# Kernel optimization log

Measured on AMD Instinct MI355X. Metric: run time of the kernel, lower is better.

Reference implementation:

```python
import jax, jax.numpy as jnp
import numpy as np

COMMITMENT_COST = 0.25
EPS = 1e-10


def setup_inputs() -> dict:
    key = jax.random.key(0)
    k1, k2 = jax.random.split(key)
    z = jax.random.normal(k1, (8, 2048, 512), dtype=jnp.float32)
    # codebook ~ small uniform init in torch; small normal is fine for a numeric reference
    codebook = jax.random.normal(k2, (4096, 512), dtype=jnp.float32) * 0.02
    return {"z": z, "codebook": codebook}


def reference(z, codebook):
    B, S, D = z.shape
    K = codebook.shape[0]
    flat_z = z.reshape(-1, D)  # [N, D]
    distances = (
        jnp.sum(flat_z * flat_z, axis=1, keepdims=True)
        + jnp.sum(codebook * codebook, axis=1)
        - 2.0 * flat_z @ codebook.T
    )
    encoding_indices = jnp.argmin(distances, axis=1)  # [N] int
    z_q = codebook[encoding_indices].reshape(z.shape)  # gather lookup
    # commitment loss (z_q detached)
    commitment_loss = jnp.mean((z - jax.lax.stop_gradient(z_q)) ** 2)
    loss = COMMITMENT_COST * commitment_loss
    # straight-through estimator
    z_q_st = z + jax.lax.stop_gradient(z_q - z)
    # perplexity from codebook usage histogram
    N = flat_z.shape[0]
    counts = jnp.zeros((K,), dtype=jnp.float32).at[encoding_indices].add(1.0)
    avg_probs = counts / N
    perplexity = jnp.exp(-jnp.sum(avg_probs * jnp.log(avg_probs + EPS)))
    encoding_indices = encoding_indices.reshape(B, S)
    return (z_q_st, loss, encoding_indices, perplexity)
```

## Files before the change

kernel.cpp:

```cpp
#include <hip/hip_runtime.h>
#include <hip/hip_fp16.h>
#include <stdint.h>

#define B_  8
#define S_  2048
#define D_  512
#define K_  4096
#define N_  (B_ * S_)
#define NCB (K_ / 128)
#define NKB32 (D_ / 32)
#define MARGIN 0.014f

typedef _Float16 half8  __attribute__((ext_vector_type(8)));
typedef float    floatx4 __attribute__((ext_vector_type(4)));

#define OFF_PK   0
#define OFF_EN   (OFF_PK + (size_t)N_ * NCB * 8)
#define OFF_ZN   (OFF_EN + K_ * 4)
#define OFF_CNT  (OFF_ZN + N_ * 4)
#define OFF_BL   (OFF_CNT + K_ * 4)
#define OFF_ZH   (OFF_BL + 4096 * 4)
#define OFF_EH   (OFF_ZH + (size_t)N_ * D_ * 2)

__device__ __forceinline__ uint32_t umin32(uint32_t a, uint32_t b) { return a < b ? a : b; }
__device__ __forceinline__ uint32_t umax32(uint32_t a, uint32_t b) { return a > b ? a : b; }
__device__ __forceinline__ bool lexlt(float va, int ia, float vb, int ib) {
    return va < vb || (va == vb && ia < ib);
}

__device__ __forceinline__ void load_lds16(const _Float16* g, _Float16* l) {
    __builtin_amdgcn_global_load_lds(
        (const __attribute__((address_space(1))) unsigned int*)(uintptr_t)g,
        (__attribute__((address_space(3))) unsigned int*)(uintptr_t)l,
        16, 0, 0);
}

__global__ __launch_bounds__(256)
void vq_prep_kernel(const float* __restrict__ z, const float* __restrict__ cb,
                    _Float16* __restrict__ zh, _Float16* __restrict__ eh,
                    float* __restrict__ znorm, float* __restrict__ enorm,
                    int* __restrict__ counts) {
    const int t = threadIdx.x;
    if (blockIdx.x < 16) counts[blockIdx.x * 256 + t] = 0;

    const size_t u = (size_t)blockIdx.x * 256 + t;
    const int c   = (int)(u & 63);
    const int row = (int)(u >> 6);
    const bool isZ = row < N_;
    const int n = isZ ? row : row - N_;
    const float* r = (isZ ? z : cb) + (size_t)n * D_;

    float s = 0.f;
    for (int j = c; j < D_; j += 64) { float v = r[j]; s += v * v; }
    #pragma unroll
    for (int m = 1; m < 64; m <<= 1) s += __shfl_xor(s, m, 64);
    if (c == 0) { if (isZ) znorm[n] = s; else enorm[n] = s; }

    const float scale = isZ ? 1.0f : 64.0f;
    const float4 v0 = *(const float4*)(r + c * 8);
    const float4 v1 = *(const float4*)(r + c * 8 + 4);
    float a[8] = {v0.x, v0.y, v0.z, v0.w, v1.x, v1.y, v1.z, v1.w};
    half8 h;
    #pragma unroll
    for (int j = 0; j < 8; j++) h[j] = (_Float16)(a[j] * scale);
    const int kb = c >> 2, qd = c & 3;
    const int sw = qd ^ ((n >> 1) & 3);
    const size_t rows = isZ ? (size_t)N_ : (size_t)K_;
    const size_t off = (size_t)kb * rows * 32 + (size_t)n * 32 + (size_t)(sw << 3);
    *(half8*)((isZ ? zh : eh) + off) = h;
}

__global__ __launch_bounds__(256, 4)
void vq_dist_kernel(const _Float16* __restrict__ zh, const _Float16* __restrict__ eh,
                    const float* __restrict__ enorm, const float* __restrict__ znorm,
                    uint2* __restrict__ pK) {
    __shared__ _Float16 sA[2][4096];
    __shared__ float sE[128], sZn[128];
    __shared__ uint2 cK[2][128];

    const int t  = threadIdx.x;
    const int c0 = blockIdx.x * 128;
    const int m0 = blockIdx.y * 128;

    if (t < 128) { sE[t] = enorm[c0 + t]; sZn[t] = znorm[m0 + t]; }

    const int lane = t & 63, wid = t >> 6;
    const int wr = wid & 1, wc = wid >> 1;
    const int qd = lane >> 4, nl = lane & 15;
    const int sw8 = (qd ^ ((nl >> 1) & 3)) << 3;

    const _Float16* gsrc = zh + (size_t)m0 * 32 + (size_t)(wid * 2) * 512 + (size_t)lane * 8;
    const size_t strideA = (size_t)N_ * 32;
    const size_t strideB = (size_t)K_ * 32;
    const _Float16* bptr = eh + (size_t)c0 * 32 + (size_t)((wc * 64 + nl) * 32 + sw8);
    const int aoff = (wr * 64 + nl) * 32 + sw8;

    floatx4 acc[4][4];
    #pragma unroll
    for (int i = 0; i < 4; i++)
        #pragma unroll
        for (int j = 0; j < 4; j++) acc[i][j] = (floatx4)0.f;

    #pragma unroll
    for (int g = 0; g < 2; g++)
        load_lds16(gsrc + g * 512, sA[0] + wid * 2 * 512 + g * 512);

    for (int kb = 0; kb < NKB32; kb++) {
        __syncthreads();

        half8 b_h[4];
        #pragma unroll
        for (int s = 0; s < 4; s++)
            b_h[s] = *(const half8*)(bptr + s * 512);
        if (kb + 1 < NKB32) {
            const _Float16* gk = gsrc + (size_t)(kb + 1) * strideA;
            _Float16* ld = sA[(kb + 1) & 1] + wid * 2 * 512;
            #pragma unroll
            for (int g = 0; g < 2; g++)
                load_lds16(gk + g * 512, ld + g * 512);
        }
        const _Float16* ah = sA[kb & 1] + aoff;
        half8 a_h[4];
        #pragma unroll
        for (int s = 0; s < 4; s++)
            a_h[s] = *(const half8*)(ah + s * 512);
        #pragma unroll
        for (int i = 0; i < 4; i++)
            #pragma unroll
            for (int j = 0; j < 4; j++)
                acc[i][j] = __builtin_amdgcn_mfma_f32_16x16x32_f16(a_h[i], b_h[j], acc[i][j], 0, 0, 0);
        bptr += strideB;
    }

    uint32_t colc[4]; float se4[4];
    #pragma unroll
    for (int sn = 0; sn < 4; sn++) {
        const int cl = wc * 64 + sn * 16 + nl;
        colc[sn] = (uint32_t)cl;
        se4[sn]  = sE[cl];
    }
    #pragma unroll
    for (int sm = 0; sm < 4; sm++) {
        #pragma unroll
        for (int reg = 0; reg < 4; reg++) {
            const int rm = wr * 64 + sm * 16 + qd * 4 + reg;
            const float zn = sZn[rm];
            uint32_t k0 = 0xFFFFFFFFu, k1 = 0xFFFFFFFFu;
            #pragma unroll
            for (int sn = 0; sn < 4; sn++) {
                const float v = fmaf(acc[sm][sn][reg], -0.03125f, zn + se4[sn]);
                const uint32_t key = (__float_as_uint(v) & 0xFFFFFF80u) | colc[sn];
                const uint32_t t1 = umax32(k0, key);
                k1 = umin32(k1, t1);
                k0 = umin32(k0, key);
            }
            #pragma unroll
            for (int msk = 1; msk <= 8; msk <<= 1) {
                const uint32_t o0 = (uint32_t)__shfl_xor((int)k0, msk, 64);
                const uint32_t o1 = (uint32_t)__shfl_xor((int)k1, msk, 64);
                const uint32_t n0 = umin32(k0, o0);
                k1 = umin32(umax32(k0, o0), umin32(k1, o1));
                k0 = n0;
            }
            if (nl == 0) { cK[wc][rm].x = k0; cK[wc][rm].y = k1; }
        }
    }
    __syncthreads();
    if (t < 128) {
        const uint2 a = cK[0][t], b = cK[1][t];
        uint2 r;
        r.x = umin32(a.x, b.x);
        r.y = umin32(umax32(a.x, b.x), umin32(a.y, b.y));
        pK[(size_t)(m0 + t) * NCB + blockIdx.x] = r;
    }
}

__global__ __launch_bounds__(256)
void vq_gather_kernel(const float* __restrict__ z, const float* __restrict__ cb,
                      const float* __restrict__ znorm, const float* __restrict__ enorm,
                      const uint2* __restrict__ pK,
                      float* __restrict__ out_zq, float* __restrict__ out_idx,
                      int* __restrict__ counts, float* __restrict__ blockLoss) {
    const int lane = threadIdx.x & 63, wid = threadIdx.x >> 6;
    const int m = blockIdx.x * 4 + wid;

    uint32_t k0 = 0xFFFFFFFFu, k1 = 0xFFFFFFFFu;
    if (lane < NCB) {
        const uint2 kk = pK[(size_t)m * NCB + lane];
        k0 = kk.x; k1 = kk.y;
    }
    uint32_t g = k0;
    #pragma unroll
    for (int msk = 1; msk < 64; msk <<= 1) {
        const uint32_t o = (uint32_t)__shfl_xor((int)g, msk, 64);
        g = umin32(g, o);
    }
    const float gvf = __uint_as_float(g & 0xFFFFFF80u) + MARGIN;
    const bool f0 = (lane < NCB) && (__uint_as_float(k0 & 0xFFFFFF80u) <= gvf);
    const bool f1 = (lane < NCB) && (__uint_as_float(k1 & 0xFFFFFF80u) <= gvf);
    const unsigned long long b0 = __ballot(f0), b1 = __ballot(f1);
    int idx;
    if (__popcll(b0) + __popcll(b1) <= 1) {
        const unsigned long long bw = __ballot(k0 == g);
        idx = (int)__builtin_ctzll(bw) * 128 + (int)(g & 0x7Fu);
    } else {
        const float zn = znorm[m];
        const float* zrow = z + (size_t)m * D_;
        float bestd = 1e30f; int besti = 0x7fffffff;
        #pragma unroll
        for (int slot = 0; slot < 2; slot++) {
            unsigned long long bm = slot ? b1 : b0;
            while (bm) {
                const int l = (int)__builtin_ctzll(bm); bm &= bm - 1;
                const uint32_t kx = (uint32_t)__shfl((int)(slot ? k1 : k0), l, 64);
                const int cand = l * 128 + (int)(kx & 0x7Fu);
                const float* crow = cb + (size_t)cand * D_;
                float s = 0.f;
                #pragma unroll
                for (int j = 0; j < 8; j++)
                    s += zrow[lane * 8 + j] * crow[lane * 8 + j];
                #pragma unroll
                for (int msk = 1; msk < 64; msk <<= 1) s += __shfl_xor(s, msk, 64);
                const float d = (zn + enorm[cand]) - 2.0f * s;
                if (lexlt(d, cand, bestd, besti)) { bestd = d; besti = cand; }
            }
        }
        idx = besti;
    }

    const float4* qrow  = (const float4*)(cb + (size_t)idx * D_);
    const float4* zrow4 = (const float4*)(z + (size_t)m * D_);
    float4*       orow  = (float4*)(out_zq + (size_t)m * D_);
    float lsum = 0.f;
    #pragma unroll
    for (int i = 0; i < 2; i++) {
        const int j = lane + i * 64;
        const float4 q  = qrow[j];
        const float4 zv = zrow4[j];
        float4 o;
        o.x = zv.x + (q.x - zv.x); o.y = zv.y + (q.y - zv.y);
        o.z = zv.z + (q.z - zv.z); o.w = zv.w + (q.w - zv.w);
        orow[j] = o;
        const float dx = zv.x - q.x, dy = zv.y - q.y, dz = zv.z - q.z, dw = zv.w - q.w;
        lsum += dx * dx + dy * dy + dz * dz + dw * dw;
    }
    #pragma unroll
    for (int msk = 1; msk < 64; msk <<= 1) lsum += __shfl_xor(lsum, msk, 64);

    if (lane == 0) {
        out_idx[m] = (float)idx;
        atomicAdd(&counts[idx], 1);
    }
    __shared__ float wl[4];
    if (lane == 0) wl[wid] = lsum;
    __syncthreads();
    if (threadIdx.x == 0) blockLoss[blockIdx.x] = wl[0] + wl[1] + wl[2] + wl[3];
}

__global__ void vq_final_kernel(const int* __restrict__ counts,
                                const float* __restrict__ blockLoss,
                                float* __restrict__ out_loss, float* __restrict__ out_ppl) {
    __shared__ float sl[256], se[256];
    const int t = threadIdx.x;
    float ls = 0.f, es = 0.f;
    for (int i = t; i < N_ / 4; i += 256) ls += blockLoss[i];
    for (int k = t; k < K_; k += 256) {
        const float p = (float)counts[k] / (float)N_;
        es += p * logf(p + 1e-10f);
    }
    sl[t] = ls; se[t] = es;
    __syncthreads();
    for (int s = 128; s > 0; s >>= 1) {
        if (t < s) { sl[t] += sl[t + s]; se[t] += se[t + s]; }
        __syncthreads();
    }
    if (t == 0) {
        out_loss[0] = 0.25f * (sl[0] / (float)((size_t)N_ * D_));
        out_ppl[0]  = expf(-se[0]);
    }
}

extern "C" void kernel_launch(void* const* d_in, const int* in_sizes, int n_in,
                              void* d_out, int out_size, void* d_ws, size_t ws_size,
                              hipStream_t stream) {
    const float* z  = (const float*)d_in[0];
    const float* cb = (const float*)d_in[1];
    float* out = (float*)d_out;

    char* ws = (char*)d_ws;
    uint2*    pK        = (uint2*)   (ws + OFF_PK);
    float*    enorm     = (float*)   (ws + OFF_EN);
    float*    znorm     = (float*)   (ws + OFF_ZN);
    int*      counts    = (int*)     (ws + OFF_CNT);
    float*    blockLoss = (float*)   (ws + OFF_BL);
    _Float16* zh        = (_Float16*)(ws + OFF_ZH);
    _Float16* eh        = (_Float16*)(ws + OFF_EH);

    float* out_zq   = out;
    float* out_loss = out + (size_t)N_ * D_;
    float* out_idx  = out_loss + 1;
    float* out_ppl  = out_idx + N_;

    vq_prep_kernel<<<(N_ + K_) * 64 / 256, 256, 0, stream>>>(z, cb, zh, eh,
                                                             znorm, enorm, counts);

    dim3 grid(K_ / 128, N_ / 128);
    vq_dist_kernel<<<grid, 256, 0, stream>>>(zh, eh, enorm, znorm, pK);

    vq_gather_kernel<<<N_ / 4, 256, 0, stream>>>(z, cb, znorm, enorm, pK,
                                                 out_zq, out_idx, counts, blockLoss);

    vq_final_kernel<<<1, 256, 0, stream>>>(counts, blockLoss, out_loss, out_ppl);
}
```

Baseline: 205.2 us.

## Enlarge distance GEMM block tile to 256x256 with 1024-thread workgroups

The distance kernel now uses 1024-thread workgroups, each covering a 256x256 tile of rows by codes instead of 128x128. The per-wave 64x64 sub-tile and MFMA loop stay the same. The larger tile lets each block share more staged z data in LDS and reduces the number of blocks. Partial top-2 keys are still written per 128-column chunk, so the layout the gather kernel reads does not change. The trade-off is fewer, larger workgroups: one workgroup per CU by launch bounds, a block-wide barrier across 16 waves every k-step, and possibly worse latency hiding or tail balance.

```diff
diff --git a/kernel.cpp b/kernel.cpp
--- a/kernel.cpp
+++ b/kernel.cpp
@@ -70,30 +70,30 @@
     *(half8*)((isZ ? zh : eh) + off) = h;
 }
 
-__global__ __launch_bounds__(256, 4)
+__global__ __launch_bounds__(1024, 1)
 void vq_dist_kernel(const _Float16* __restrict__ zh, const _Float16* __restrict__ eh,
                     const float* __restrict__ enorm, const float* __restrict__ znorm,
                     uint2* __restrict__ pK) {
-    __shared__ _Float16 sA[2][4096];
-    __shared__ float sE[128], sZn[128];
-    __shared__ uint2 cK[2][128];
+    __shared__ __align__(16) _Float16 sA[2][8192];
+    __shared__ float sE[256], sZn[256];
+    __shared__ uint2 cK[4][256];
 
     const int t  = threadIdx.x;
-    const int c0 = blockIdx.x * 128;
-    const int m0 = blockIdx.y * 128;
-
-    if (t < 128) { sE[t] = enorm[c0 + t]; sZn[t] = znorm[m0 + t]; }
+    const int c0 = blockIdx.x * 256;
+    const int m0 = blockIdx.y * 256;
+
+    if (t < 256) { sE[t] = enorm[c0 + t]; sZn[t] = znorm[m0 + t]; }
 
     const int lane = t & 63, wid = t >> 6;
-    const int wr = wid & 1, wc = wid >> 1;
+    const int wrow = wid & 3, wcol = wid >> 2;
     const int qd = lane >> 4, nl = lane & 15;
     const int sw8 = (qd ^ ((nl >> 1) & 3)) << 3;
 
-    const _Float16* gsrc = zh + (size_t)m0 * 32 + (size_t)(wid * 2) * 512 + (size_t)lane * 8;
     const size_t strideA = (size_t)N_ * 32;
     const size_t strideB = (size_t)K_ * 32;
-    const _Float16* bptr = eh + (size_t)c0 * 32 + (size_t)((wc * 64 + nl) * 32 + sw8);
-    const int aoff = (wr * 64 + nl) * 32 + sw8;
+    const _Float16* gsrc = zh + (size_t)m0 * 32 + (size_t)t * 8;
+    const _Float16* bptr = eh + (size_t)c0 * 32 + (size_t)((wcol * 64 + nl) * 32 + sw8);
+    const int aoff = (wrow * 64 + nl) * 32 + sw8;
 
     floatx4 acc[4][4];
     #pragma unroll
@@ -101,24 +101,18 @@
         #pragma unroll
         for (int j = 0; j < 4; j++) acc[i][j] = (floatx4)0.f;
 
-    #pragma unroll
-    for (int g = 0; g < 2; g++)
-        load_lds16(gsrc + g * 512, sA[0] + wid * 2 * 512 + g * 512);
+    load_lds16(gsrc, sA[0] + t * 8);
 
     for (int kb = 0; kb < NKB32; kb++) {
         __syncthreads();
 
+        const _Float16* bp = bptr + (size_t)kb * strideB;
         half8 b_h[4];
         #pragma unroll
         for (int s = 0; s < 4; s++)
-            b_h[s] = *(const half8*)(bptr + s * 512);
-        if (kb + 1 < NKB32) {
-            const _Float16* gk = gsrc + (size_t)(kb + 1) * strideA;
-            _Float16* ld = sA[(kb + 1) & 1] + wid * 2 * 512;
-            #pragma unroll
-            for (int g = 0; g < 2; g++)
-                load_lds16(gk + g * 512, ld + g * 512);
-        }
+            b_h[s] = *(const half8*)(bp + s * 512);
+        if (kb + 1 < NKB32)
+            load_lds16(gsrc + (size_t)(kb + 1) * strideA, sA[(kb + 1) & 1] + t * 8);
         const _Float16* ah = sA[kb & 1] + aoff;
         half8 a_h[4];
         #pragma unroll
@@ -129,21 +123,20 @@
             #pragma unroll
             for (int j = 0; j < 4; j++)
                 acc[i][j] = __builtin_amdgcn_mfma_f32_16x16x32_f16(a_h[i], b_h[j], acc[i][j], 0, 0, 0);
-        bptr += strideB;
     }
 
     uint32_t colc[4]; float se4[4];
     #pragma unroll
     for (int sn = 0; sn < 4; sn++) {
-        const int cl = wc * 64 + sn * 16 + nl;
+        const int cl = (wcol & 1) * 64 + sn * 16 + nl;
         colc[sn] = (uint32_t)cl;
-        se4[sn]  = sE[cl];
+        se4[sn]  = sE[wcol * 64 + sn * 16 + nl];
     }
     #pragma unroll
     for (int sm = 0; sm < 4; sm++) {
         #pragma unroll
         for (int reg = 0; reg < 4; reg++) {
-            const int rm = wr * 64 + sm * 16 + qd * 4 + reg;
+            const int rm = wrow * 64 + sm * 16 + qd * 4 + reg;
             const float zn = sZn[rm];
             uint32_t k0 = 0xFFFFFFFFu, k1 = 0xFFFFFFFFu;
             #pragma unroll
@@ -162,16 +155,17 @@
                 k1 = umin32(umax32(k0, o0), umin32(k1, o1));
                 k0 = n0;
             }
-            if (nl == 0) { cK[wc][rm].x = k0; cK[wc][rm].y = k1; }
+            if (nl == 0) { cK[wcol][rm].x = k0; cK[wcol][rm].y = k1; }
         }
     }
     __syncthreads();
-    if (t < 128) {
-        const uint2 a = cK[0][t], b = cK[1][t];
+    if (t < 512) {
+        const int row = t & 255, h = t >> 8;
+        const uint2 a = cK[2 * h][row], b = cK[2 * h + 1][row];
         uint2 r;
         r.x = umin32(a.x, b.x);
         r.y = umin32(umax32(a.x, b.x), umin32(a.y, b.y));
-        pK[(size_t)(m0 + t) * NCB + blockIdx.x] = r;
+        pK[(size_t)(m0 + row) * NCB + blockIdx.x * 2 + h] = r;
     }
 }
 
@@ -304,8 +298,8 @@
     vq_prep_kernel<<<(N_ + K_) * 64 / 256, 256, 0, stream>>>(z, cb, zh, eh,
                                                              znorm, enorm, counts);
 
-    dim3 grid(K_ / 128, N_ / 128);
-    vq_dist_kernel<<<grid, 256, 0, stream>>>(zh, eh, enorm, znorm, pK);
+    dim3 grid(K_ / 256, N_ / 256);
+    vq_dist_kernel<<<grid, 1024, 0, stream>>>(zh, eh, enorm, znorm, pK);
 
     vq_gather_kernel<<<N_ / 4, 256, 0, stream>>>(z, cb, znorm, enorm, pK,
                                                  out_zq, out_idx, counts, blockLoss);
```

New measurement: 216.3 us. 5.4% more time.
